# Performance work log

Hardware: AMD Instinct MI355X
Metric: run time of the kernel (lower is better)

Reference implementation:

```python
import jax, jax.numpy as jnp
import numpy as np

EPS = 1e-12  # torch F.normalize eps


def _unfold(x, k, pad, stride):
    # torch F.unfold: [B,C,H,W] -> [B, C*k*k, L], channel-major then kernel (i,j)
    B, C, H, W = x.shape
    xp = jnp.pad(x, ((0, 0), (0, 0), (pad, pad), (pad, pad)))
    Ho = (H + 2 * pad - k) // stride + 1
    Wo = (W + 2 * pad - k) // stride + 1
    patches = [xp[:, :, i:i + stride * (Ho - 1) + 1:stride, j:j + stride * (Wo - 1) + 1:stride]
               for i in range(k) for j in range(k)]
    p = jnp.stack(patches, axis=2)  # [B, C, k*k, Ho, Wo]
    return p.reshape(B, C * k * k, Ho * Wo)


def _fold(t, out_hw, k, pad, stride):
    # torch F.fold: [B, C*k*k, L] -> [B, C, H, W] with overlap-add
    B, Ckk, L = t.shape
    C = Ckk // (k * k)
    H, W = out_hw
    Ho = (H + 2 * pad - k) // stride + 1
    Wo = (W + 2 * pad - k) // stride + 1
    t = t.reshape(B, C, k, k, Ho, Wo)
    out = jnp.zeros((B, C, H + 2 * pad, W + 2 * pad), t.dtype)
    for i in range(k):
        for j in range(k):
            out = out.at[:, :, i:i + stride * (Ho - 1) + 1:stride,
                         j:j + stride * (Wo - 1) + 1:stride].add(t[:, :, i, j])
    return out[:, :, pad:pad + H, pad:pad + W]


def setup_inputs() -> dict:
    key = jax.random.key(0)
    ks = jax.random.split(key, 5)
    B, C3, H3 = 4, 256, 48
    return {
        'dh_img_lv3': jax.random.normal(ks[0], (B, C3, H3, H3), jnp.float32),
        'dh_ref_lv3': jax.random.normal(ks[1], (B, C3, H3, H3), jnp.float32),
        'cl_ref_lv1': jax.random.normal(ks[2], (B, 64, H3 * 4, H3 * 4), jnp.float32),
        'cl_ref_lv2': jax.random.normal(ks[3], (B, 128, H3 * 2, H3 * 2), jnp.float32),
        'cl_ref_lv3': jax.random.normal(ks[4], (B, C3, H3, H3), jnp.float32),
    }


def reference(dh_img_lv3, dh_ref_lv3, cl_ref_lv1, cl_ref_lv2, cl_ref_lv3):
    ksz, pad = 3, 1
    B, C3, H3, W3 = dh_img_lv3.shape

    q = _unfold(dh_img_lv3, ksz, pad, 1)                      # [B, D, Lq]
    kmat = _unfold(dh_ref_lv3, ksz, pad, 1).transpose(0, 2, 1)  # [B, Lk, D]
    kmat = kmat / jnp.maximum(jnp.linalg.norm(kmat, axis=2, keepdims=True), EPS)
    q = q / jnp.maximum(jnp.linalg.norm(q, axis=1, keepdims=True), EPS)

    rel = jnp.einsum('bld,bdm->blm', kmat, q)                 # [B, Lk, Lq]
    rel_val = jnp.max(rel, axis=1, keepdims=True)             # [B, 1, Lq]  (top-1, k=1)
    rel_idx = jnp.argmax(rel, axis=1, keepdims=True)          # [B, 1, Lq]

    v3 = _unfold(cl_ref_lv3, ksz, pad, 1)                     # [B, C3*9,   Lk]
    v2 = _unfold(cl_ref_lv2, 2 * ksz, 2 * pad, 2)             # [B, C2*36,  Lk]
    v1 = _unfold(cl_ref_lv1, 4 * ksz, 4 * pad, 4)             # [B, C1*144, Lk]

    def transfer(v):
        idx = jnp.broadcast_to(rel_idx, (B, v.shape[1], rel_idx.shape[2]))
        tv = jnp.take_along_axis(v, idx, axis=2)              # [B, Cv, Lq]
        # weighted sum over k=1 topk / sum of weights (faithful to original)
        return (rel_val * tv) / rel_val

    T3u, T2u, T1u = transfer(v3), transfer(v2), transfer(v1)

    def fold_norm(Tu, scale, k_, p_, s_):
        hw = (H3 * scale, W3 * scale)
        cnt = _fold(jnp.ones_like(Tu), hw, k_, p_, s_)
        return _fold(Tu, hw, k_, p_, s_) / cnt

    T_lv3 = fold_norm(T3u, 1, ksz, pad, 1)
    T_lv2 = fold_norm(T2u, 2, 2 * ksz, 2 * pad, 2)
    T_lv1 = fold_norm(T1u, 4, 4 * ksz, 4 * pad, 4)

    S = rel_val.reshape(B, 1, H3, W3)
    return S, T_lv3, T_lv2, T_lv1
```

## Files before the change

### kernel.cpp

```cpp
#include <hip/hip_runtime.h>


#define HW3 2304
#define PLANE 589824
#define MP 2560
#define KP 512

typedef __bf16 v8bf __attribute__((ext_vector_type(8)));
typedef float v16f __attribute__((ext_vector_type(16)));

#define O_PSI  0
#define O_PSR  9216
#define O_IKN  18432
#define O_IQN  27648
#define O_RIDX 36864
#define O_IKNP 46080
#define O_CAND 56320
#define O_CANDV 93184
#define O_IMGT 130048
#define O_REFT 2489344
#define O_APL  4848640
#define O_BPL  7470080
#define O_U    10091520

__global__ __launch_bounds__(256) void k_pixsq(const float* __restrict__ img,
                                               const float* __restrict__ ref,
                                               float* __restrict__ psi,
                                               float* __restrict__ psr) {
  __shared__ float ri[4][64], rr[4][64];
  const int t = threadIdx.x, lane = t & 63, cg = t >> 6;
  const int pix = blockIdx.x * 64 + lane;
  const int b = pix / HW3, p = pix - b * HW3;
  const float* ib = img + (size_t)b * PLANE + p;
  const float* rb = ref + (size_t)b * PLANE + p;
  float si = 0.f, sr = 0.f;
#pragma unroll 8
  for (int c = 0; c < 64; ++c) {
    float x = ib[(cg * 64 + c) * HW3]; si = fmaf(x, x, si);
    float y = rb[(cg * 64 + c) * HW3]; sr = fmaf(y, y, sr);
  }
  ri[cg][lane] = si; rr[cg][lane] = sr;
  __syncthreads();
  if (t < 64) {
    float a = ri[0][t] + ri[1][t] + ri[2][t] + ri[3][t];
    float s2 = rr[0][t] + rr[1][t] + rr[2][t] + rr[3][t];
    psi[blockIdx.x * 64 + t] = a; psr[blockIdx.x * 64 + t] = s2;
  }
}

__global__ __launch_bounds__(256) void k_norm(const float* __restrict__ psr,
                                              const float* __restrict__ psi,
                                              float* __restrict__ ikn,
                                              float* __restrict__ iqn) {
  int pix = blockIdx.x * 256 + threadIdx.x;
  int b = pix / HW3, p = pix - b * HW3;
  int py = p / 48, px = p - py * 48;
  float sr = 0.f, si = 0.f;
#pragma unroll
  for (int dy = -1; dy <= 1; ++dy)
#pragma unroll
    for (int dx = -1; dx <= 1; ++dx) {
      if (py + dy < 0 || py + dy >= 48 || px + dx < 0 || px + dx >= 48) continue;
      int n = pix + dy * 48 + dx;
      sr += psr[n]; si += psi[n];
    }
  ikn[pix] = 1.0f / fmaxf(sqrtf(sr), 1e-12f);
  iqn[pix] = 1.0f / fmaxf(sqrtf(si), 1e-12f);
}

__global__ __launch_bounds__(256) void k_normp(const float* __restrict__ psr,
                                               float* __restrict__ iknp) {
  int idx = blockIdx.x * 256 + threadIdx.x;
  int b = idx / MP, pp = idx - b * MP;
  int py = pp / 50, px = pp - py * 50;
  float r = __uint_as_float(0x7fc00000u);
  if (pp < 2500 && py != 0 && py != 49 && px != 0 && px != 49) {
    int y = py - 1, x = px - 1;
    float s = 0.f;
    for (int dy = -1; dy <= 1; ++dy)
      for (int dx = -1; dx <= 1; ++dx) {
        int yy = y + dy, xx = x + dx;
        if (yy >= 0 && yy < 48 && xx >= 0 && xx < 48)
          s += psr[b * HW3 + yy * 48 + xx];
      }
    r = 1.0f / fmaxf(sqrtf(s), 1e-12f);
  }
  iknp[idx] = r;
}

__global__ __launch_bounds__(256) void k_padsplit(const float* __restrict__ src,
                                                  __bf16* __restrict__ dst) {
  __shared__ float sm[64][65];
  const int pix0 = blockIdx.x * 64, c0 = blockIdx.y * 64, b = blockIdx.z;
  const int lane = threadIdx.x & 63, q4 = threadIdx.x >> 6;
  const float* s = src + (size_t)b * PLANE;
#pragma unroll
  for (int r = 0; r < 16; ++r) {
    int cl = r * 4 + q4;
    sm[cl][lane] = s[(size_t)(c0 + cl) * HW3 + pix0 + lane];
  }
  __syncthreads();
  __bf16* d = dst + (size_t)b * MP * KP;
#pragma unroll
  for (int r = 0; r < 16; ++r) {
    int pl = r * 4 + q4;
    int p = pix0 + pl;
    int py = p / 48, px = p - py * 48;
    int pp = (py + 1) * 50 + px + 1;
    float v = sm[lane][pl];
    __bf16 hi = (__bf16)v;
    __bf16 lo = (__bf16)(v - (float)hi);
    d[(size_t)pp * KP + c0 + lane] = hi;
    d[(size_t)pp * KP + 256 + c0 + lane] = lo;
  }
}

__global__ __launch_bounds__(256) void k_tr(const float* __restrict__ src,
                                            float* __restrict__ dst,
                                            int C, int HW, int b0) {
  __shared__ float sm[64][65];
  int pix0 = blockIdx.x * 64, c0 = blockIdx.y * 64;
  const float* s = src + (size_t)(b0 + blockIdx.z) * C * HW;
  float* d = dst + (size_t)blockIdx.z * HW * C;
  int lane = threadIdx.x & 63, q4 = threadIdx.x >> 6;
#pragma unroll
  for (int r = 0; r < 16; ++r) {
    int cl = r * 4 + q4;
    sm[cl][lane] = s[(size_t)(c0 + cl) * HW + pix0 + lane];
  }
  __syncthreads();
#pragma unroll
  for (int r = 0; r < 16; ++r) {
    int pl = r * 4 + q4;
    d[(size_t)(pix0 + pl) * C + c0 + lane] = sm[lane][pl];
  }
}

__global__ __launch_bounds__(256) void k_gemm_u(const __bf16* __restrict__ Apl,
                                                const __bf16* __restrict__ Bpl,
                                                float* __restrict__ U, int b0) {
  __shared__ __align__(16) char smem[36864];
  __bf16 (*As)[72] = (__bf16(*)[72])smem;
  __bf16 (*Bs)[72] = (__bf16(*)[72])(smem + 18432);
  const int b = b0 + blockIdx.z;
  const __bf16* Ab = Apl + (size_t)b * MP * KP;
  const __bf16* Bb = Bpl + (size_t)b * MP * KP;
  float* Ub = U + (size_t)blockIdx.z * (2560LL * 2560LL);
  const int t = threadIdx.x;
  const int q0 = blockIdx.y * 126 - 1, p0 = blockIdx.x * 126 - 1;
  const int lane = t & 63, w = t >> 6, wr = w >> 1, wc = w & 1;
  const int sr = t >> 1, ss = (t & 1) * 32;
  const int l31 = lane & 31, kb = (lane >> 5) * 8;
  const int arow = q0 + sr, brow = p0 + sr;
  const bool aok = (unsigned)arow < 2560u, bok = (unsigned)brow < 2560u;

  v16f acc[2][2];
#pragma unroll
  for (int i = 0; i < 2; ++i)
#pragma unroll
    for (int j = 0; j < 2; ++j)
#pragma unroll
      for (int e = 0; e < 16; ++e) acc[i][j][e] = 0.f;

  const float4 z4 = make_float4(0.f, 0.f, 0.f, 0.f);
  for (int kv = 0; kv < 768; kv += 64) {
    const int ak = kv < 256 ? kv : kv - 256;
    const int bk = kv < 512 ? kv : kv - 512;
    const __bf16* ga = Ab + (size_t)arow * KP + ak + ss;
    const __bf16* gb = Bb + (size_t)brow * KP + bk + ss;
    float4 a0 = aok ? *(const float4*)(ga)      : z4;
    float4 a1 = aok ? *(const float4*)(ga + 8)  : z4;
    float4 a2 = aok ? *(const float4*)(ga + 16) : z4;
    float4 a3 = aok ? *(const float4*)(ga + 24) : z4;
    float4 b0v = bok ? *(const float4*)(gb)      : z4;
    float4 b1v = bok ? *(const float4*)(gb + 8)  : z4;
    float4 b2v = bok ? *(const float4*)(gb + 16) : z4;
    float4 b3v = bok ? *(const float4*)(gb + 24) : z4;
    __syncthreads();
    *(float4*)(&As[sr][ss])      = a0;
    *(float4*)(&As[sr][ss + 8])  = a1;
    *(float4*)(&As[sr][ss + 16]) = a2;
    *(float4*)(&As[sr][ss + 24]) = a3;
    *(float4*)(&Bs[sr][ss])      = b0v;
    *(float4*)(&Bs[sr][ss + 8])  = b1v;
    *(float4*)(&Bs[sr][ss + 16]) = b2v;
    *(float4*)(&Bs[sr][ss + 24]) = b3v;
    __syncthreads();
#pragma unroll
    for (int kk = 0; kk < 4; ++kk) {
      const int ko = kk * 16 + kb;
      v8bf af0 = *(const v8bf*)(&As[wr * 64 + l31][ko]);
      v8bf af1 = *(const v8bf*)(&As[wr * 64 + 32 + l31][ko]);
      v8bf bg0 = *(const v8bf*)(&Bs[wc * 64 + l31][ko]);
      v8bf bg1 = *(const v8bf*)(&Bs[wc * 64 + 32 + l31][ko]);
      acc[0][0] = __builtin_amdgcn_mfma_f32_32x32x16_bf16(af0, bg0, acc[0][0], 0, 0, 0);
      acc[0][1] = __builtin_amdgcn_mfma_f32_32x32x16_bf16(af0, bg1, acc[0][1], 0, 0, 0);
      acc[1][0] = __builtin_amdgcn_mfma_f32_32x32x16_bf16(af1, bg0, acc[1][0], 0, 0, 0);
      acc[1][1] = __builtin_amdgcn_mfma_f32_32x32x16_bf16(af1, bg1, acc[1][1], 0, 0, 0);
    }
  }

  float (*Sd)[128] = (float(*)[128])smem;
#pragma unroll
  for (int h = 0; h < 2; ++h) {
    const int rlo = h * 63;
    __syncthreads();
#pragma unroll
    for (int mf = 0; mf < 2; ++mf)
#pragma unroll
      for (int nf = 0; nf < 2; ++nf) {
        const int col = wc * 64 + nf * 32 + l31;
#pragma unroll
        for (int r16 = 0; r16 < 16; ++r16) {
          const int row = wr * 64 + mf * 32 + (r16 & 3) + 8 * (r16 >> 2) + 4 * (lane >> 5);
          const int lr = row - rlo;
          if (lr >= 0 && lr < 65) Sd[lr][col] = acc[mf][nf][r16];
        }
      }
    __syncthreads();
    for (int idx = t; idx < 63 * 126; idx += 256) {
      const int lr = idx / 126 + 1;
      const int ce = idx - (lr - 1) * 126 + 1;
      const int gq = q0 + rlo + lr;
      const int gp = p0 + ce;
      if ((unsigned)gq < 2560u && (unsigned)gp < 2560u)
        Ub[(size_t)gq * 2560 + gp] = Sd[lr - 1][ce - 1] + Sd[lr][ce] + Sd[lr + 1][ce + 1];
    }
  }
}

__global__ __launch_bounds__(256) void k_argmax_u(const float* __restrict__ U,
                                                  const float* __restrict__ iknp,
                                                  int* __restrict__ cand,
                                                  float* __restrict__ candv, int b0) {
  __shared__ float Lu[24][356];
  __shared__ float smv[16][4][2];
  __shared__ int   smi[16][4][2];
  const int zb = blockIdx.z >> 1, half = blockIdx.z & 1;
  const int b = b0 + zb;
  const float* Ub = U + (size_t)zb * (2560LL * 2560LL);
  const int qy0 = blockIdx.y * 4, qx0 = blockIdx.x * 4;
  const int kb = half * 1280;
  const int t = threadIdx.x, lane = t & 63, wv = t >> 6;

  float b1[16], b2[16]; int i1[16], i2[16];
#pragma unroll
  for (int i = 0; i < 16; ++i) { b1[i] = -3e38f; b2[i] = -3e38f; i1[i] = 0x3fffffff; i2[i] = 0x3fffffff; }

  for (int ch = 0; ch < 5; ++ch) {
    const int kc = kb + ch * 256;
    for (int rr = wv; rr < 24; rr += 4) {
      const int g = rr >> 2, a = rr & 3;
      const float* src = Ub + (size_t)((qy0 + g) * 50 + qx0 + 1 + a) * 2560;
      float* dst = Lu[rr];
      for (int c = lane; c < 356; c += 64) {
        const int gc = kc - 50 + c;
        dst[c] = ((unsigned)gc < 2560u) ? src[gc] : 0.f;
      }
    }
    __syncthreads();
    const float ikv = iknp[b * MP + kc + t];
    const int p = kc + t;
#pragma unroll
    for (int e = 0; e < 4; ++e)
#pragma unroll
      for (int a = 0; a < 4; ++a) {
        const float rel = Lu[e * 4 + a][t] + Lu[(e + 1) * 4 + a][t + 50] + Lu[(e + 2) * 4 + a][t + 100];
        const float v = rel * ikv;
        const int qi = e * 4 + a;
        if (v > b1[qi]) { b2[qi] = b1[qi]; i2[qi] = i1[qi]; b1[qi] = v; i1[qi] = p; }
        else if (v > b2[qi]) { b2[qi] = v; i2[qi] = p; }
      }
    __syncthreads();
  }

#pragma unroll
  for (int qi = 0; qi < 16; ++qi) {
    float x1 = b1[qi], x2 = b2[qi]; int j1 = i1[qi], j2 = i2[qi];
#pragma unroll
    for (int off = 32; off; off >>= 1) {
      float o1 = __shfl_down(x1, off), o2 = __shfl_down(x2, off);
      int oj1 = __shfl_down(j1, off), oj2 = __shfl_down(j2, off);
      if (o1 > x1 || (o1 == x1 && oj1 < j1)) {
        float tv = x1; int tj = j1;
        x1 = o1; j1 = oj1;
        if (o2 > tv || (o2 == tv && oj2 < tj)) { x2 = o2; j2 = oj2; }
        else { x2 = tv; j2 = tj; }
      } else if (o1 > x2 || (o1 == x2 && oj1 < j2)) { x2 = o1; j2 = oj1; }
    }
    if (lane == 0) { smv[qi][wv][0] = x1; smv[qi][wv][1] = x2; smi[qi][wv][0] = j1; smi[qi][wv][1] = j2; }
  }
  __syncthreads();
  if (t < 16) {
    float x1 = smv[t][0][0], x2 = smv[t][0][1]; int j1 = smi[t][0][0], j2 = smi[t][0][1];
#pragma unroll
    for (int w2 = 1; w2 < 4; ++w2) {
      float o1 = smv[t][w2][0], o2 = smv[t][w2][1];
      int oj1 = smi[t][w2][0], oj2 = smi[t][w2][1];
      if (o1 > x1 || (o1 == x1 && oj1 < j1)) {
        float tv = x1; int tj = j1;
        x1 = o1; j1 = oj1;
        if (o2 > tv || (o2 == tv && oj2 < tj)) { x2 = o2; j2 = oj2; }
        else { x2 = tv; j2 = tj; }
      } else if (o1 > x2 || (o1 == x2 && oj1 < j2)) { x2 = o1; j2 = oj1; }
    }
    int my1 = j1 / 50, my2 = j2 / 50;
    int m1 = (my1 - 1) * 48 + (j1 - my1 * 50 - 1);
    int m2 = (my2 - 1) * 48 + (j2 - my2 * 50 - 1);
    const int q = (qy0 + (t >> 2)) * 48 + qx0 + (t & 3);
    const size_t base = ((size_t)b * HW3 + q) * 4 + half * 2;
    cand[base] = m1; cand[base + 1] = m2;
    candv[base] = x1; candv[base + 1] = x2;
  }
}

__global__ __launch_bounds__(256) void k_pick(const float* __restrict__ imgT,
                                              const float* __restrict__ refT,
                                              const float* __restrict__ ikn,
                                              const float* __restrict__ iqn,
                                              const int* __restrict__ cand,
                                              const float* __restrict__ candv,
                                              int* __restrict__ ridx,
                                              float* __restrict__ outS) {
  const int t = threadIdx.x, lane = t & 63, wv = t >> 6;
  const int qg = blockIdx.x * 4 + wv;
  const int b = qg / HW3, q = qg - b * HW3;
  int ci[4]; float cv[4];
#pragma unroll
  for (int s = 0; s < 4; ++s) { ci[s] = cand[(size_t)qg * 4 + s]; cv[s] = candv[(size_t)qg * 4 + s]; }
  int o1 = 0;
#pragma unroll
  for (int s = 1; s < 4; ++s)
    if (cv[s] > cv[o1] || (cv[s] == cv[o1] && ci[s] < ci[o1])) o1 = s;
  int o2 = -1;
#pragma unroll
  for (int s = 0; s < 4; ++s) {
    if (s == o1) continue;
    if (o2 < 0 || cv[s] > cv[o2] || (cv[s] == cv[o2] && ci[s] < ci[o2])) o2 = s;
  }
  int m1 = ci[o1], m2 = ci[o2];
  float v1 = cv[o1], v2 = cv[o2];
  int win = m1; float wval = v1;
  if (v1 - v2 <= 1e-5f * fmaxf(fabsf(v1), 1.0f)) {
    const int qy = q / 48, qx = q - qy * 48;
    const float* iT = imgT + (size_t)b * HW3 * 256;
    const float* rT = refT + (size_t)b * HW3 * 256;
    const int p1y = m1 / 48, p1x = m1 - p1y * 48;
    const int p2y = m2 / 48, p2x = m2 - p2y * 48;
    float s1 = 0.f, s2 = 0.f;
    for (int dy = -1; dy <= 1; ++dy) {
      int yq = qy + dy; if (yq < 0 || yq >= 48) continue;
      for (int dx = -1; dx <= 1; ++dx) {
        int xq = qx + dx; if (xq < 0 || xq >= 48) continue;
        const float* qrow = iT + (size_t)(yq * 48 + xq) * 256;
        int y1 = p1y + dy, x1 = p1x + dx, y2 = p2y + dy, x2 = p2x + dx;
        bool k1 = (y1 >= 0 && y1 < 48 && x1 >= 0 && x1 < 48);
        bool k2 = (y2 >= 0 && y2 < 48 && x2 >= 0 && x2 < 48);
        const float* r1 = rT + (size_t)(k1 ? y1 * 48 + x1 : 0) * 256;
        const float* r2 = rT + (size_t)(k2 ? y2 * 48 + x2 : 0) * 256;
#pragma unroll
        for (int j = 0; j < 4; ++j) {
          float qv = qrow[lane + j * 64];
          if (k1) s1 = fmaf(qv, r1[lane + j * 64], s1);
          if (k2) s2 = fmaf(qv, r2[lane + j * 64], s2);
        }
      }
    }
#pragma unroll
    for (int off = 32; off; off >>= 1) {
      s1 += __shfl_down(s1, off);
      s2 += __shfl_down(s2, off);
    }
    float e1 = s1 * ikn[b * HW3 + m1], e2 = s2 * ikn[b * HW3 + m2];
    if (e2 > e1 || (e2 == e1 && m2 < m1)) { win = m2; wval = e2; }
    else { win = m1; wval = e1; }
  }
  if (lane == 0) {
    ridx[b * HW3 + q] = win;
    outS[qg] = wval * iqn[b * HW3 + q];
  }
}

__global__ __launch_bounds__(256) void k_foldgather(const float* __restrict__ t,
                                                    const int* __restrict__ ridx,
                                                    float* __restrict__ out,
                                                    int C, int H, int sc, int b0) {
  __shared__ int   soff[64][9];
  __shared__ float sicnt[64];
  __shared__ float tr[64][65];
  const int HW = H * H;
  const int b = b0 + blockIdx.y;
  const float* tb = t + (size_t)blockIdx.y * HW * C;
  const int* rb = ridx + b * HW3;
  const int pix0 = blockIdx.x * 64;

  for (int e = threadIdx.x; e < 576; e += 256) {
    int op = e / 9, tap = e - op * 9;
    int pix = pix0 + op;
    int h = pix / H, w = pix - h * H;
    int hi = h / sc, hr = h - hi * sc;
    int wi = w / sc, wr = w - wi * sc;
    int ii = tap / 3, jj = tap - ii * 3;
    int oy = hi + 1 - ii, ox = wi + 1 - jj;
    int off = -1;
    if (oy >= 0 && oy < 48 && ox >= 0 && ox < 48) {
      int m = rb[oy * 48 + ox];
      int my = m / 48, mx = m - my * 48;
      int y = sc * (my - 1 + ii) + hr;
      int x = sc * (mx - 1 + jj) + wr;
      if (y >= 0 && y < H && x >= 0 && x < H) off = y * H + x;
    }
    soff[op][tap] = off;
    if (tap == 0) {
      int cnt = 0;
#pragma unroll
      for (int i2 = 0; i2 < 3; ++i2)
#pragma unroll
        for (int j2 = 0; j2 < 3; ++j2) {
          int oy2 = hi + 1 - i2, ox2 = wi + 1 - j2;
          if (oy2 >= 0 && oy2 < 48 && ox2 >= 0 && ox2 < 48) ++cnt;
        }
      sicnt[op] = 1.0f / (float)cnt;
    }
  }
  __syncthreads();

  const int g = threadIdx.x >> 6, lane = threadIdx.x & 63;
  for (int c0 = 0; c0 < C; c0 += 64) {
#pragma unroll
    for (int o = 0; o < 16; ++o) {
      int op = g * 16 + o;
      float s = 0.f;
#pragma unroll
      for (int tp = 0; tp < 9; ++tp) {
        int off = soff[op][tp];
        if (off >= 0) s += tb[(size_t)off * C + c0 + lane];
      }
      tr[op][lane] = s * sicnt[op];
    }
    __syncthreads();
#pragma unroll
    for (int r = 0; r < 16; ++r) {
      int cl = r * 4 + g;
      out[((size_t)b * C + c0 + cl) * HW + pix0 + lane] = tr[lane][cl];
    }
    __syncthreads();
  }
}

extern "C" void kernel_launch(void* const* d_in, const int* in_sizes, int n_in,
                              void* d_out, int out_size, void* d_ws, size_t ws_size,
                              hipStream_t stream) {
  (void)in_sizes; (void)n_in; (void)out_size;
  const float* img = (const float*)d_in[0];
  const float* ref = (const float*)d_in[1];
  const float* cl1 = (const float*)d_in[2];
  const float* cl2 = (const float*)d_in[3];
  const float* cl3 = (const float*)d_in[4];
  float* out = (float*)d_out;

  float* ws   = (float*)d_ws;
  float* ps_i = ws + O_PSI;
  float* ps_r = ws + O_PSR;
  float* ikn  = ws + O_IKN;
  float* iqn  = ws + O_IQN;
  int*   ridx = (int*)(ws + O_RIDX);
  float* iknp = ws + O_IKNP;
  int*   cand = (int*)(ws + O_CAND);
  float* candv = ws + O_CANDV;
  float* imgT = ws + O_IMGT;
  float* refT = ws + O_REFT;
  __bf16* Apl = (__bf16*)(ws + O_APL);
  __bf16* Bpl = (__bf16*)(ws + O_BPL);
  float* Um   = ws + O_U;

  hipMemsetAsync(ws + O_APL, 0, (size_t)(O_U - O_APL) * 4, stream);

  k_pixsq<<<144, 256, 0, stream>>>(img, ref, ps_i, ps_r);
  k_norm<<<36, 256, 0, stream>>>(ps_r, ps_i, ikn, iqn);
  k_normp<<<40, 256, 0, stream>>>(ps_r, iknp);
  k_padsplit<<<dim3(36, 4, 4), 256, 0, stream>>>(img, Apl);
  k_padsplit<<<dim3(36, 4, 4), 256, 0, stream>>>(ref, Bpl);
  k_tr<<<dim3(36, 4, 4), 256, 0, stream>>>(img, imgT, 256, HW3, 0);
  k_tr<<<dim3(36, 4, 4), 256, 0, stream>>>(ref, refT, 256, HW3, 0);

  const long long UPF = 2560LL * 2560LL;
  const long long availf = (long long)(ws_size / 4) - O_U;
  const int nb = (availf >= 4 * UPF) ? 4 : ((availf >= 2 * UPF) ? 2 : 1);
  for (int g = 0; g < 4; g += nb) {
    k_gemm_u<<<dim3(21, 21, nb), 256, 0, stream>>>(Apl, Bpl, Um, g);
    k_argmax_u<<<dim3(12, 12, nb * 2), 256, 0, stream>>>(Um, iknp, cand, candv, g);
  }
  k_pick<<<2304, 256, 0, stream>>>(imgT, refT, ikn, iqn, cand, candv, ridx, out);

  float* t = ws + O_IMGT;
  k_tr<<<dim3(36, 4, 4), 256, 0, stream>>>(cl3, t, 256, 2304, 0);
  k_foldgather<<<dim3(36, 4), 256, 0, stream>>>(t, ridx, out + 9216, 256, 48, 1, 0);
  k_tr<<<dim3(144, 2, 4), 256, 0, stream>>>(cl2, t, 128, 9216, 0);
  k_foldgather<<<dim3(144, 4), 256, 0, stream>>>(t, ridx, out + 2368512, 128, 96, 2, 0);
  k_tr<<<dim3(576, 1, 4), 256, 0, stream>>>(cl1, t, 64, 36864, 0);
  k_foldgather<<<dim3(576, 4), 256, 0, stream>>>(t, ridx, out + 7087104, 64, 192, 4, 0);
}
```

Before: 885.8 us.

## Split argmax over five key ranges and read U directly without LDS staging

```diff
diff --git a/kernel.cpp b/kernel.cpp
--- a/kernel.cpp
+++ b/kernel.cpp
@@ -16,12 +16,12 @@
 #define O_RIDX 36864
 #define O_IKNP 46080
 #define O_CAND 56320
-#define O_CANDV 93184
-#define O_IMGT 130048
-#define O_REFT 2489344
-#define O_APL  4848640
-#define O_BPL  7470080
-#define O_U    10091520
+#define O_CANDV 148480
+#define O_IMGT 240640
+#define O_REFT 2599936
+#define O_APL  4959232
+#define O_BPL  7580672
+#define O_U    10202112
 
 __global__ __launch_bounds__(256) void k_pixsq(const float* __restrict__ img,
                                                const float* __restrict__ ref,
@@ -229,49 +229,54 @@
   }
 }
 
-__global__ __launch_bounds__(256) void k_argmax_u(const float* __restrict__ U,
+__device__ __forceinline__ void top2merge(float& b1, int& i1, float& b2, int& i2,
+                                          float o1, int oj1, float o2, int oj2) {
+  if (o1 > b1 || (o1 == b1 && oj1 < i1)) {
+    float t1 = b1; int tj = i1;
+    b1 = o1; i1 = oj1;
+    if (o2 > t1 || (o2 == t1 && oj2 < tj)) { b2 = o2; i2 = oj2; }
+    else { b2 = t1; i2 = tj; }
+  } else if (o1 > b2 || (o1 == b2 && oj1 < i2)) {
+    b2 = o1; i2 = oj1;
+  }
+}
+
+__global__ __launch_bounds__(256) void k_argmax_d(const float* __restrict__ U,
                                                   const float* __restrict__ iknp,
                                                   int* __restrict__ cand,
                                                   float* __restrict__ candv, int b0) {
-  __shared__ float Lu[24][356];
   __shared__ float smv[16][4][2];
   __shared__ int   smi[16][4][2];
-  const int zb = blockIdx.z >> 1, half = blockIdx.z & 1;
+  const int zb = blockIdx.z / 5, split = blockIdx.z - zb * 5;
   const int b = b0 + zb;
   const float* Ub = U + (size_t)zb * (2560LL * 2560LL);
   const int qy0 = blockIdx.y * 4, qx0 = blockIdx.x * 4;
-  const int kb = half * 1280;
+  const int Q0 = (qy0 + 1) * 50 + qx0 + 1;
   const int t = threadIdx.x, lane = t & 63, wv = t >> 6;
 
   float b1[16], b2[16]; int i1[16], i2[16];
 #pragma unroll
   for (int i = 0; i < 16; ++i) { b1[i] = -3e38f; b2[i] = -3e38f; i1[i] = 0x3fffffff; i2[i] = 0x3fffffff; }
 
-  for (int ch = 0; ch < 5; ++ch) {
-    const int kc = kb + ch * 256;
-    for (int rr = wv; rr < 24; rr += 4) {
-      const int g = rr >> 2, a = rr & 3;
-      const float* src = Ub + (size_t)((qy0 + g) * 50 + qx0 + 1 + a) * 2560;
-      float* dst = Lu[rr];
-      for (int c = lane; c < 356; c += 64) {
-        const int gc = kc - 50 + c;
-        dst[c] = ((unsigned)gc < 2560u) ? src[gc] : 0.f;
-      }
-    }
-    __syncthreads();
-    const float ikv = iknp[b * MP + kc + t];
-    const int p = kc + t;
+#pragma unroll
+  for (int cc = 0; cc < 2; ++cc) {
+    const int P0 = split * 512 + cc * 256;
+    const int p = P0 + t;
+    const float ikv = iknp[b * MP + p];
+    const float* baseP = Ub + (size_t)Q0 * 2560 + p;
 #pragma unroll
     for (int e = 0; e < 4; ++e)
 #pragma unroll
       for (int a = 0; a < 4; ++a) {
-        const float rel = Lu[e * 4 + a][t] + Lu[(e + 1) * 4 + a][t + 50] + Lu[(e + 2) * 4 + a][t + 100];
-        const float v = rel * ikv;
+        const ptrdiff_t o = (ptrdiff_t)(50 * e + a) * 2560;
+        const float vm = baseP[o - 50 * 2560 - 50];
+        const float v0 = baseP[o];
+        const float vp = baseP[o + 50 * 2560 + 50];
+        const float v = (vm + v0 + vp) * ikv;
         const int qi = e * 4 + a;
         if (v > b1[qi]) { b2[qi] = b1[qi]; i2[qi] = i1[qi]; b1[qi] = v; i1[qi] = p; }
         else if (v > b2[qi]) { b2[qi] = v; i2[qi] = p; }
       }
-    __syncthreads();
   }
 
 #pragma unroll
@@ -281,12 +286,7 @@
     for (int off = 32; off; off >>= 1) {
       float o1 = __shfl_down(x1, off), o2 = __shfl_down(x2, off);
       int oj1 = __shfl_down(j1, off), oj2 = __shfl_down(j2, off);
-      if (o1 > x1 || (o1 == x1 && oj1 < j1)) {
-        float tv = x1; int tj = j1;
-        x1 = o1; j1 = oj1;
-        if (o2 > tv || (o2 == tv && oj2 < tj)) { x2 = o2; j2 = oj2; }
-        else { x2 = tv; j2 = tj; }
-      } else if (o1 > x2 || (o1 == x2 && oj1 < j2)) { x2 = o1; j2 = oj1; }
+      top2merge(x1, j1, x2, j2, o1, oj1, o2, oj2);
     }
     if (lane == 0) { smv[qi][wv][0] = x1; smv[qi][wv][1] = x2; smi[qi][wv][0] = j1; smi[qi][wv][1] = j2; }
   }
@@ -294,21 +294,13 @@
   if (t < 16) {
     float x1 = smv[t][0][0], x2 = smv[t][0][1]; int j1 = smi[t][0][0], j2 = smi[t][0][1];
 #pragma unroll
-    for (int w2 = 1; w2 < 4; ++w2) {
-      float o1 = smv[t][w2][0], o2 = smv[t][w2][1];
-      int oj1 = smi[t][w2][0], oj2 = smi[t][w2][1];
-      if (o1 > x1 || (o1 == x1 && oj1 < j1)) {
-        float tv = x1; int tj = j1;
-        x1 = o1; j1 = oj1;
-        if (o2 > tv || (o2 == tv && oj2 < tj)) { x2 = o2; j2 = oj2; }
-        else { x2 = tv; j2 = tj; }
-      } else if (o1 > x2 || (o1 == x2 && oj1 < j2)) { x2 = o1; j2 = oj1; }
-    }
+    for (int w2 = 1; w2 < 4; ++w2)
+      top2merge(x1, j1, x2, j2, smv[t][w2][0], smi[t][w2][0], smv[t][w2][1], smi[t][w2][1]);
     int my1 = j1 / 50, my2 = j2 / 50;
     int m1 = (my1 - 1) * 48 + (j1 - my1 * 50 - 1);
     int m2 = (my2 - 1) * 48 + (j2 - my2 * 50 - 1);
     const int q = (qy0 + (t >> 2)) * 48 + qx0 + (t & 3);
-    const size_t base = ((size_t)b * HW3 + q) * 4 + half * 2;
+    const size_t base = ((size_t)b * HW3 + q) * 10 + split * 2;
     cand[base] = m1; cand[base + 1] = m2;
     candv[base] = x1; candv[base + 1] = x2;
   }
@@ -325,21 +317,17 @@
   const int t = threadIdx.x, lane = t & 63, wv = t >> 6;
   const int qg = blockIdx.x * 4 + wv;
   const int b = qg / HW3, q = qg - b * HW3;
-  int ci[4]; float cv[4];
-#pragma unroll
-  for (int s = 0; s < 4; ++s) { ci[s] = cand[(size_t)qg * 4 + s]; cv[s] = candv[(size_t)qg * 4 + s]; }
-  int o1 = 0;
-#pragma unroll
-  for (int s = 1; s < 4; ++s)
-    if (cv[s] > cv[o1] || (cv[s] == cv[o1] && ci[s] < ci[o1])) o1 = s;
-  int o2 = -1;
-#pragma unroll
-  for (int s = 0; s < 4; ++s) {
-    if (s == o1) continue;
-    if (o2 < 0 || cv[s] > cv[o2] || (cv[s] == cv[o2] && ci[s] < ci[o2])) o2 = s;
-  }
-  int m1 = ci[o1], m2 = ci[o2];
-  float v1 = cv[o1], v2 = cv[o2];
+  int m1 = 0, m2 = 0; float v1 = -3e38f, v2 = -3e38f;
+#pragma unroll
+  for (int s = 0; s < 10; ++s) {
+    int ci = cand[(size_t)qg * 10 + s];
+    float cv = candv[(size_t)qg * 10 + s];
+    if (cv > v1 || (cv == v1 && ci < m1)) {
+      float tv = v1; int tj = m1;
+      v1 = cv; m1 = ci;
+      if (tv > v2 || (tv == v2 && tj < m2)) { v2 = tv; m2 = tj; }
+    } else if (cv > v2 || (cv == v2 && ci < m2)) { v2 = cv; m2 = ci; }
+  }
   int win = m1; float wval = v1;
   if (v1 - v2 <= 1e-5f * fmaxf(fabsf(v1), 1.0f)) {
     const int qy = q / 48, qx = q - qy * 48;
@@ -489,7 +477,7 @@
   const int nb = (availf >= 4 * UPF) ? 4 : ((availf >= 2 * UPF) ? 2 : 1);
   for (int g = 0; g < 4; g += nb) {
     k_gemm_u<<<dim3(21, 21, nb), 256, 0, stream>>>(Apl, Bpl, Um, g);
-    k_argmax_u<<<dim3(12, 12, nb * 2), 256, 0, stream>>>(Um, iknp, cand, candv, g);
+    k_argmax_d<<<dim3(12, 12, nb * 5), 256, 0, stream>>>(Um, iknp, cand, candv, g);
   }
   k_pick<<<2304, 256, 0, stream>>>(imgT, refT, ikn, iqn, cand, candv, ridx, out);
 
```

Measured after the change: 757.2 us. 14.5% less time.
